# Kernel optimization log

Measured on AMD Instinct MI355X. Metric: run time of the kernel, lower is better.

Reference implementation:

```python
import jax, jax.numpy as jnp
import numpy as np

N = 20000   # nodes
E = 320000  # edges (before self-loops)
HID = 64    # hidden_dim
H = 4       # attention heads
C = HID     # per-head channels (concat=False -> mean over heads)
CDIM = 8    # contrastive_dim
NEG_SLOPE = 0.2


def setup_inputs() -> dict:
    key = jax.random.key(0)
    ks = jax.random.split(key, 32)
    g = lambda k, shape: (jax.random.normal(k, shape, jnp.float32) * 0.05)
    inp = {
        "x": jax.random.normal(ks[0], (N, 8), jnp.float32),
        "edge_index": jax.random.randint(ks[1], (2, E), 0, N, jnp.int64),
        # lc_encode MLP: 8 -> 32 -> HID
        "W_enc1": g(ks[2], (8, 32)),  "b_enc1": jnp.zeros((32,), jnp.float32),
        "W_enc2": g(ks[3], (32, HID)), "b_enc2": jnp.zeros((HID,), jnp.float32),
        # three GATConv layers: lin (HID -> H*C, no bias), att_src/att_dst (H, C), bias (C,)
        "W_g1": g(ks[4], (HID, H * C)), "as1": g(ks[5], (H, C)), "ad1": g(ks[6], (H, C)), "bg1": jnp.zeros((C,), jnp.float32),
        "W_g2": g(ks[7], (HID, H * C)), "as2": g(ks[8], (H, C)), "ad2": g(ks[9], (H, C)), "bg2": jnp.zeros((C,), jnp.float32),
        "W_g3": g(ks[10], (HID, H * C)), "as3": g(ks[11], (H, C)), "ad3": g(ks[12], (H, C)), "bg3": jnp.zeros((C,), jnp.float32),
        # output MLP: HID -> 64 -> 32 -> CDIM (dropout inactive at eval)
        "W_o1": g(ks[13], (HID, 64)), "b_o1": jnp.zeros((64,), jnp.float32),
        "W_o2": g(ks[14], (64, 32)),  "b_o2": jnp.zeros((32,), jnp.float32),
        "W_o3": g(ks[15], (32, CDIM)), "b_o3": jnp.zeros((CDIM,), jnp.float32),
    }
    return inp


def gat_conv(x, src, dst, n, W, att_src, att_dst, bias):
    # PyG GATConv, heads=H, concat=False (mean over heads), eval mode (no dropout)
    h = (x @ W).reshape(n, H, C)                       # [N,H,C]
    a_src = jnp.einsum('nhc,hc->nh', h, att_src)        # [N,H]
    a_dst = jnp.einsum('nhc,hc->nh', h, att_dst)        # [N,H]
    logits = jax.nn.leaky_relu(a_src[src] + a_dst[dst], NEG_SLOPE)  # [Etot,H]
    m = jax.ops.segment_max(logits, dst, num_segments=n)            # segment softmax (stable)
    e = jnp.exp(logits - m[dst])
    denom = jax.ops.segment_sum(e, dst, num_segments=n)
    alpha = e / (denom[dst] + 1e-16)                    # [Etot,H]
    msg = h[src] * alpha[:, :, None]                    # [Etot,H,C]
    out = jax.ops.segment_sum(msg, dst, num_segments=n) # [N,H,C]
    return out.mean(axis=1) + bias                      # concat=False -> head mean


def reference(x, edge_index, W_enc1, b_enc1, W_enc2, b_enc2,
              W_g1, as1, ad1, bg1, W_g2, as2, ad2, bg2, W_g3, as3, ad3, bg3,
              W_o1, b_o1, W_o2, b_o2, W_o3, b_o3):
    n = x.shape[0]
    loops = jnp.arange(n, dtype=edge_index.dtype)       # GATConv add_self_loops=True
    src = jnp.concatenate([edge_index[0], loops])
    dst = jnp.concatenate([edge_index[1], loops])

    h = jax.nn.elu(jax.nn.elu(x @ W_enc1 + b_enc1) @ W_enc2 + b_enc2)
    h1 = gat_conv(h, src, dst, n, W_g1, as1, ad1, bg1) + h
    h2 = gat_conv(h1, src, dst, n, W_g2, as2, ad2, bg2) + h1
    h3 = gat_conv(h2, src, dst, n, W_g3, as3, ad3, bg3) + h2

    o = jax.nn.elu(h3 @ W_o1 + b_o1)
    o = jax.nn.elu(o @ W_o2 + b_o2)
    return o @ W_o3 + b_o3
```

## Files before the change

kernel.cpp:

```cpp
#include <hip/hip_runtime.h>
#include <cstdint>
#include <cstddef>

#define NEG_SLOPE 0.2f

__device__ __forceinline__ float elu_f(float x) {
    return x > 0.f ? x : expm1f(x);
}

__global__ __launch_bounds__(256) void prep_kernel(
    const int* __restrict__ ei,
    const float* __restrict__ W0, const float* __restrict__ as0, const float* __restrict__ ad0,
    const float* __restrict__ W1, const float* __restrict__ as1, const float* __restrict__ ad1,
    const float* __restrict__ W2, const float* __restrict__ as2, const float* __restrict__ ad2,
    int* __restrict__ cnt, int* __restrict__ ready, int* __restrict__ flag,
    float* __restrict__ vfold, int n) {
    const int b = blockIdx.x, t = threadIdx.x;
    if (b < 79) {
        const int i = b * 256 + t;
        if (i < n) cnt[i] = 0;
        if (b == 0) {
            if (t < 128) ready[t] = 0;
            if (t == 0) {
                int acc = 0;
#pragma unroll
                for (int k = 0; k < 8; ++k) acc |= ei[2 * k + 1];
                flag[0] = (acc == 0) ? 1 : 0;
            }
        }
        return;
    }
    const int e = (b - 79) * 256 + t;
    if (e >= 1536) return;
    const int l = e >> 9, rem = e & 511;
    const int k = rem >> 3, j = rem & 7, h = j & 3;
    const float* W   = (l == 0) ? W0  : (l == 1) ? W1  : W2;
    const float* as_ = (l == 0) ? as0 : (l == 1) ? as1 : as2;
    const float* ad_ = (l == 0) ? ad0 : (l == 1) ? ad1 : ad2;
    const float* av = (j < 4) ? as_ : ad_;
    const float* wr = W + k * 256 + h * 64;
    const float* ar = av + h * 64;
    float s = 0.f;
#pragma unroll 8
    for (int cc = 0; cc < 64; ++cc) s += wr[cc] * ar[cc];
    vfold[l * 512 + k * 8 + j] = s;
}

__global__ void count_kernel(const int* __restrict__ ei, const int* __restrict__ flag,
                             int E, int Etot, int* __restrict__ cnt) {
    int e = blockIdx.x * blockDim.x + threadIdx.x;
    if (e >= Etot) return;
    int d;
    if (e < E) d = flag[0] ? ei[2 * (size_t)(E + e)] : ei[E + e];
    else       d = e - E;
    atomicAdd(&cnt[d], 1);
}

#define SCAN_B 256
__global__ __launch_bounds__(256) void scan_onepass_kernel(
    const int* __restrict__ cnt, int* __restrict__ ready,
    int* __restrict__ rowptr, int* __restrict__ cursor, int n) {
    __shared__ int sd[SCAN_B];
    __shared__ int sred[128];
    __shared__ int s_pref;
    const int b = blockIdx.x, t = threadIdx.x;
    const int g = b * SCAN_B + t;
    const int v = (g < n) ? cnt[g] : 0;
    sd[t] = v;
    __syncthreads();
    for (int off = 1; off < SCAN_B; off <<= 1) {
        int add = (t >= off) ? sd[t - off] : 0;
        __syncthreads();
        sd[t] += add;
        __syncthreads();
    }
    if (t == SCAN_B - 1) atomicExch(&ready[b], sd[SCAN_B - 1] + 1);
    if (t < 128) {
        int pv = 0;
        if (t < b) {
            do { pv = atomicAdd(&ready[t], 0); __builtin_amdgcn_s_sleep(1); } while (pv == 0);
            pv -= 1;
        }
        sred[t] = pv;
    }
    __syncthreads();
    if (t == 0) {
        int s = 0;
#pragma unroll 8
        for (int i = 0; i < 128; ++i) s += sred[i];
        s_pref = s;
    }
    __syncthreads();
    const int pre = s_pref;
    if (g < n) {
        const int e = pre + sd[t];
        rowptr[g + 1] = e;
        cursor[g] = e - v;
        if (g == 0) rowptr[0] = 0;
    }
}

__global__ void fill_kernel(const int* __restrict__ ei, const int* __restrict__ flag,
                            int E, int Etot, int* __restrict__ cursor,
                            int* __restrict__ col) {
    int e = blockIdx.x * blockDim.x + threadIdx.x;
    if (e >= Etot) return;
    int s, d;
    if (e < E) {
        if (flag[0]) { s = ei[2 * (size_t)e]; d = ei[2 * (size_t)(E + e)]; }
        else         { s = ei[e];             d = ei[E + e]; }
    } else {
        s = d = e - E;
    }
    int pos = atomicAdd(&cursor[d], 1);
    col[pos] = s;
}

#define H1STR 68
__global__ __launch_bounds__(256) void encoder_kernel(
    const float* __restrict__ x,
    const float* __restrict__ W1, const float* __restrict__ b1,
    const float* __restrict__ W2, const float* __restrict__ b2,
    const float* __restrict__ vfold0,
    float* __restrict__ h0, float* __restrict__ asrc, float* __restrict__ adst,
    int n_nodes) {
    __shared__ float W1s[256];
    __shared__ float b1s[32];
    __shared__ float W2s[2048];
    __shared__ float b2s[64];
    __shared__ float vsd[512];
    __shared__ float xS[512];
    __shared__ float h1T[32 * H1STR];
    const int t = threadIdx.x;
    const int n0 = blockIdx.x * 64;
    const int rem = n_nodes - n0;

    *(float4*)(W2s + t * 4) = *(const float4*)(W2 + t * 4);
    *(float4*)(W2s + 1024 + t * 4) = *(const float4*)(W2 + 1024 + t * 4);
    if (t < 64)  *(float4*)(W1s + t * 4) = *(const float4*)(W1 + t * 4);
    if (t < 8)   *(float4*)(b1s + t * 4) = *(const float4*)(b1 + t * 4);
    if (t < 16)  *(float4*)(b2s + t * 4) = *(const float4*)(b2 + t * 4);
    if (t < 128) *(float4*)(vsd + t * 4) = *(const float4*)(vfold0 + t * 4);
    if (t < 128) {
        const int fidx = t * 4;
        float4 v = make_float4(0.f, 0.f, 0.f, 0.f);
        if (fidx < rem * 8) v = *(const float4*)(x + (size_t)n0 * 8 + fidx);
        *(float4*)(xS + fidx) = v;
    }
    __syncthreads();

    {
        const int nl = t >> 2;
        const int j0 = (t & 3) * 8;
        const float4 xa = *(const float4*)(xS + nl * 8);
        const float4 xb = *(const float4*)(xS + nl * 8 + 4);
        const float xk[8] = {xa.x, xa.y, xa.z, xa.w, xb.x, xb.y, xb.z, xb.w};
        float a[8];
#pragma unroll
        for (int u = 0; u < 8; ++u) a[u] = b1s[j0 + u];
#pragma unroll
        for (int k = 0; k < 8; ++k) {
            const float4 w0 = *(const float4*)(W1s + k * 32 + j0);
            const float4 w1 = *(const float4*)(W1s + k * 32 + j0 + 4);
            a[0] += xk[k] * w0.x; a[1] += xk[k] * w0.y;
            a[2] += xk[k] * w0.z; a[3] += xk[k] * w0.w;
            a[4] += xk[k] * w1.x; a[5] += xk[k] * w1.y;
            a[6] += xk[k] * w1.z; a[7] += xk[k] * w1.w;
        }
#pragma unroll
        for (int u = 0; u < 8; ++u) h1T[(j0 + u) * H1STR + nl] = elu_f(a[u]);
    }
    __syncthreads();

    const int cg = t & 15;
    const int nq = t >> 4;
    const int c0 = cg * 4;
    float acc[4][4];
#pragma unroll
    for (int i = 0; i < 4; ++i)
#pragma unroll
        for (int c = 0; c < 4; ++c) acc[i][c] = b2s[c0 + c];
#pragma unroll 8
    for (int k = 0; k < 32; ++k) {
        const float4 hv = *(const float4*)(h1T + k * H1STR + nq * 4);
        const float4 wv = *(const float4*)(W2s + k * 64 + c0);
        const float hvv[4] = {hv.x, hv.y, hv.z, hv.w};
#pragma unroll
        for (int i = 0; i < 4; ++i) {
            acc[i][0] += hvv[i] * wv.x; acc[i][1] += hvv[i] * wv.y;
            acc[i][2] += hvv[i] * wv.z; acc[i][3] += hvv[i] * wv.w;
        }
    }
    float o[4][4];
#pragma unroll
    for (int i = 0; i < 4; ++i)
#pragma unroll
        for (int c = 0; c < 4; ++c) o[i][c] = elu_f(acc[i][c]);

#pragma unroll
    for (int i = 0; i < 4; ++i) {
        const int n = n0 + nq * 4 + i;
        if (n < n_nodes)
            *(float4*)(h0 + (size_t)n * 64 + c0) =
                make_float4(o[i][0], o[i][1], o[i][2], o[i][3]);
    }
    float ad[4][8];
#pragma unroll
    for (int i = 0; i < 4; ++i)
#pragma unroll
        for (int jj = 0; jj < 8; ++jj) ad[i][jj] = 0.f;
#pragma unroll
    for (int c = 0; c < 4; ++c) {
        const float4 v0 = *(const float4*)(vsd + (c0 + c) * 8);
        const float4 v1 = *(const float4*)(vsd + (c0 + c) * 8 + 4);
#pragma unroll
        for (int i = 0; i < 4; ++i) {
            ad[i][0] += o[i][c] * v0.x; ad[i][1] += o[i][c] * v0.y;
            ad[i][2] += o[i][c] * v0.z; ad[i][3] += o[i][c] * v0.w;
            ad[i][4] += o[i][c] * v1.x; ad[i][5] += o[i][c] * v1.y;
            ad[i][6] += o[i][c] * v1.z; ad[i][7] += o[i][c] * v1.w;
        }
    }
#pragma unroll
    for (int off = 1; off < 16; off <<= 1) {
#pragma unroll
        for (int i = 0; i < 4; ++i)
#pragma unroll
            for (int jj = 0; jj < 8; ++jj)
                ad[i][jj] += __shfl_xor(ad[i][jj], off);
    }
    if (cg == 0) {
#pragma unroll
        for (int i = 0; i < 4; ++i) {
            const int n = n0 + nq * 4 + i;
            if (n < n_nodes) {
#pragma unroll
                for (int h = 0; h < 4; ++h) {
                    asrc[n * 4 + h] = ad[i][h];
                    adst[n * 4 + h] = ad[i][4 + h];
                }
            }
        }
    }
}

__global__ __launch_bounds__(256) void gat_agg_kernel(
    const float* __restrict__ bin, const float* __restrict__ asrc,
    const float* __restrict__ adst, const int* __restrict__ rowptr,
    const int* __restrict__ col, float* __restrict__ g, int n_nodes) {
    const int grp = threadIdx.x >> 4;
    const int q = threadIdx.x & 15;
    const int n = blockIdx.x * 16 + grp;
    if (n >= n_nodes) return;
    const float4 ad4 = *(const float4*)(adst + (size_t)n * 4);
    const int start = rowptr[n], end = rowptr[n + 1];

    float acc[4][4];
#pragma unroll
    for (int h = 0; h < 4; ++h)
#pragma unroll
        for (int z = 0; z < 4; ++z) acc[h][z] = 0.f;
    float4 den4 = make_float4(0.f, 0.f, 0.f, 0.f);

    for (int base = start; base < end; base += 16) {
        const int cnt = min(16, end - base);
        int c = 0;
        float4 w4 = make_float4(0.f, 0.f, 0.f, 0.f);
        if (base + q < end) {
            c = col[base + q];
            const float4 av = *(const float4*)(asrc + (size_t)c * 4);
            float l0 = av.x + ad4.x; l0 = l0 > 0.f ? l0 : NEG_SLOPE * l0;
            float l1 = av.y + ad4.y; l1 = l1 > 0.f ? l1 : NEG_SLOPE * l1;
            float l2 = av.z + ad4.z; l2 = l2 > 0.f ? l2 : NEG_SLOPE * l2;
            float l3 = av.w + ad4.w; l3 = l3 > 0.f ? l3 : NEG_SLOPE * l3;
            w4.x = __expf(fminf(l0, 60.f));
            w4.y = __expf(fminf(l1, 60.f));
            w4.z = __expf(fminf(l2, 60.f));
            w4.w = __expf(fminf(l3, 60.f));
            den4.x += w4.x; den4.y += w4.y; den4.z += w4.z; den4.w += w4.w;
        }
        int j = 0;
        for (; j + 4 <= cnt; j += 4) {
#pragma unroll
            for (int u = 0; u < 4; ++u) {
                const int s = __shfl(c, j + u, 16);
                const float4 hv = *(const float4*)(bin + (size_t)s * 64 + q * 4);
                const float wx = __shfl(w4.x, j + u, 16);
                const float wy = __shfl(w4.y, j + u, 16);
                const float wz = __shfl(w4.z, j + u, 16);
                const float ww = __shfl(w4.w, j + u, 16);
                acc[0][0] += wx * hv.x; acc[0][1] += wx * hv.y;
                acc[0][2] += wx * hv.z; acc[0][3] += wx * hv.w;
                acc[1][0] += wy * hv.x; acc[1][1] += wy * hv.y;
                acc[1][2] += wy * hv.z; acc[1][3] += wy * hv.w;
                acc[2][0] += wz * hv.x; acc[2][1] += wz * hv.y;
                acc[2][2] += wz * hv.z; acc[2][3] += wz * hv.w;
                acc[3][0] += ww * hv.x; acc[3][1] += ww * hv.y;
                acc[3][2] += ww * hv.z; acc[3][3] += ww * hv.w;
            }
        }
        for (; j < cnt; ++j) {
            const int s = __shfl(c, j, 16);
            const float4 hv = *(const float4*)(bin + (size_t)s * 64 + q * 4);
            const float wx = __shfl(w4.x, j, 16);
            const float wy = __shfl(w4.y, j, 16);
            const float wz = __shfl(w4.z, j, 16);
            const float ww = __shfl(w4.w, j, 16);
            acc[0][0] += wx * hv.x; acc[0][1] += wx * hv.y;
            acc[0][2] += wx * hv.z; acc[0][3] += wx * hv.w;
            acc[1][0] += wy * hv.x; acc[1][1] += wy * hv.y;
            acc[1][2] += wy * hv.z; acc[1][3] += wy * hv.w;
            acc[2][0] += wz * hv.x; acc[2][1] += wz * hv.y;
            acc[2][2] += wz * hv.z; acc[2][3] += wz * hv.w;
            acc[3][0] += ww * hv.x; acc[3][1] += ww * hv.y;
            acc[3][2] += ww * hv.z; acc[3][3] += ww * hv.w;
        }
    }
#pragma unroll
    for (int off = 1; off < 16; off <<= 1) {
        den4.x += __shfl_xor(den4.x, off, 16);
        den4.y += __shfl_xor(den4.y, off, 16);
        den4.z += __shfl_xor(den4.z, off, 16);
        den4.w += __shfl_xor(den4.w, off, 16);
    }
    const float i0 = 1.f / (den4.x + 1e-16f);
    const float i1 = 1.f / (den4.y + 1e-16f);
    const float i2 = 1.f / (den4.z + 1e-16f);
    const float i3 = 1.f / (den4.w + 1e-16f);
    float* gr = g + (size_t)n * 256 + q * 4;
    *(float4*)(gr +   0) = make_float4(acc[0][0]*i0, acc[0][1]*i0, acc[0][2]*i0, acc[0][3]*i0);
    *(float4*)(gr +  64) = make_float4(acc[1][0]*i1, acc[1][1]*i1, acc[1][2]*i1, acc[1][3]*i1);
    *(float4*)(gr + 128) = make_float4(acc[2][0]*i2, acc[2][1]*i2, acc[2][2]*i2, acc[2][3]*i2);
    *(float4*)(gr + 192) = make_float4(acc[3][0]*i3, acc[3][1]*i3, acc[3][2]*i3, acc[3][3]*i3);
}

#define GSTR 132
__global__ __launch_bounds__(256) void gat_post_kernel(
    const float* __restrict__ g, const float* __restrict__ W,
    const float* __restrict__ bias, const float* __restrict__ xin,
    const float* __restrict__ vfold_next, int has_next,
    float* __restrict__ out, float* __restrict__ asrc, float* __restrict__ adst,
    const float* __restrict__ Wm1, const float* __restrict__ bm1,
    const float* __restrict__ Wm2, const float* __restrict__ bm2,
    const float* __restrict__ Wm3, const float* __restrict__ bm3,
    float* __restrict__ mlp_out, int n_nodes) {
    __shared__ float gS[64 * GSTR];
    __shared__ float Wp[128 * 64];
    __shared__ float vN[512];
    const int t = threadIdx.x;
    const int n0 = blockIdx.x * 64;
    const int cg = t & 7;
    const int ng = t >> 3;

    if (has_next && t < 128) *(float4*)(vN + t * 4) = *(const float4*)(vfold_next + t * 4);

    float acc[2][8];
#pragma unroll
    for (int i = 0; i < 2; ++i)
#pragma unroll
        for (int qq = 0; qq < 8; ++qq) acc[i][qq] = 0.f;

    for (int slab = 0; slab < 2; ++slab) {
        __syncthreads();
#pragma unroll
        for (int j = 0; j < 8; ++j) {
            const int idx = j * 256 + t;
            const int nl = idx >> 5;
            const int c4 = idx & 31;
            float4 v = make_float4(0.f, 0.f, 0.f, 0.f);
            if (n0 + nl < n_nodes)
                v = *(const float4*)(g + (size_t)(n0 + nl) * 256 + slab * 128 + c4 * 4);
            *(float4*)(gS + nl * GSTR + c4 * 4) = v;
        }
#pragma unroll
        for (int j = 0; j < 8; ++j) {
            const int f4 = j * 256 + t;
            const int kl = f4 >> 4;
            const int kap = slab * 128 + kl;
            const int h = kap >> 6, kk = kap & 63;
            const int c = (f4 & 15) * 4;
            *(float4*)(Wp + kl * 64 + c) = *(const float4*)(W + kk * 256 + h * 64 + c);
        }
        __syncthreads();
#pragma unroll 4
        for (int kl = 0; kl < 128; ++kl) {
            const float a0 = gS[(ng * 2 + 0) * GSTR + kl];
            const float a1 = gS[(ng * 2 + 1) * GSTR + kl];
            const float4 b0 = *(const float4*)(Wp + kl * 64 + cg * 8);
            const float4 b1 = *(const float4*)(Wp + kl * 64 + cg * 8 + 4);
            acc[0][0] += a0 * b0.x; acc[0][1] += a0 * b0.y;
            acc[0][2] += a0 * b0.z; acc[0][3] += a0 * b0.w;
            acc[0][4] += a0 * b1.x; acc[0][5] += a0 * b1.y;
            acc[0][6] += a0 * b1.z; acc[0][7] += a0 * b1.w;
            acc[1][0] += a1 * b0.x; acc[1][1] += a1 * b0.y;
            acc[1][2] += a1 * b0.z; acc[1][3] += a1 * b0.w;
            acc[1][4] += a1 * b1.x; acc[1][5] += a1 * b1.y;
            acc[1][6] += a1 * b1.z; acc[1][7] += a1 * b1.w;
        }
    }

    const int c0 = cg * 8;
    const float4 bb0 = *(const float4*)(bias + c0);
    const float4 bb1 = *(const float4*)(bias + c0 + 4);
    float o[2][8];
#pragma unroll
    for (int i = 0; i < 2; ++i) {
        const int n = n0 + ng * 2 + i;
        if (n < n_nodes) {
            const float4 x0 = *(const float4*)(xin + (size_t)n * 64 + c0);
            const float4 x1 = *(const float4*)(xin + (size_t)n * 64 + c0 + 4);
            o[i][0] = 0.25f * acc[i][0] + bb0.x + x0.x;
            o[i][1] = 0.25f * acc[i][1] + bb0.y + x0.y;
            o[i][2] = 0.25f * acc[i][2] + bb0.z + x0.z;
            o[i][3] = 0.25f * acc[i][3] + bb0.w + x0.w;
            o[i][4] = 0.25f * acc[i][4] + bb1.x + x1.x;
            o[i][5] = 0.25f * acc[i][5] + bb1.y + x1.y;
            o[i][6] = 0.25f * acc[i][6] + bb1.z + x1.z;
            o[i][7] = 0.25f * acc[i][7] + bb1.w + x1.w;
            if (has_next) {
                *(float4*)(out + (size_t)n * 64 + c0) =
                    make_float4(o[i][0], o[i][1], o[i][2], o[i][3]);
                *(float4*)(out + (size_t)n * 64 + c0 + 4) =
                    make_float4(o[i][4], o[i][5], o[i][6], o[i][7]);
            }
        } else {
#pragma unroll
            for (int qq = 0; qq < 8; ++qq) o[i][qq] = 0.f;
        }
    }

    if (has_next) {
        float pj[2][8];
#pragma unroll
        for (int i = 0; i < 2; ++i)
#pragma unroll
            for (int jj = 0; jj < 8; ++jj) pj[i][jj] = 0.f;
#pragma unroll
        for (int cidx = 0; cidx < 8; ++cidx) {
#pragma unroll
            for (int jj = 0; jj < 8; ++jj) {
                const float vv = vN[(c0 + cidx) * 8 + jj];
                pj[0][jj] += o[0][cidx] * vv;
                pj[1][jj] += o[1][cidx] * vv;
            }
        }
#pragma unroll
        for (int off = 1; off < 8; off <<= 1) {
#pragma unroll
            for (int i = 0; i < 2; ++i)
#pragma unroll
                for (int jj = 0; jj < 8; ++jj)
                    pj[i][jj] += __shfl_xor(pj[i][jj], off);
        }
        if (cg == 0) {
#pragma unroll
            for (int i = 0; i < 2; ++i) {
                const int n = n0 + ng * 2 + i;
                if (n < n_nodes) {
#pragma unroll
                    for (int h = 0; h < 4; ++h) {
                        asrc[n * 4 + h] = pj[i][h];
                        adst[n * 4 + h] = pj[i][4 + h];
                    }
                }
            }
        }
        return;
    }

    __syncthreads();
#pragma unroll
    for (int i = 0; i < 2; ++i) {
        const int nl = ng * 2 + i;
        *(float4*)(gS + nl * GSTR + c0)     = make_float4(o[i][0], o[i][1], o[i][2], o[i][3]);
        *(float4*)(gS + nl * GSTR + c0 + 4) = make_float4(o[i][4], o[i][5], o[i][6], o[i][7]);
    }
    {
#pragma unroll
        for (int j = 0; j < 4; ++j)
            *(float4*)(Wp + (j * 256 + t) * 4) = *(const float4*)(Wm1 + (j * 256 + t) * 4);
#pragma unroll
        for (int j = 0; j < 2; ++j)
            *(float4*)(Wp + 4096 + (j * 256 + t) * 4) = *(const float4*)(Wm2 + (j * 256 + t) * 4);
        if (t < 64) vN[t] = bm1[t];
        else if (t < 96) vN[t] = bm2[t - 64];
        else if (t < 104) vN[t] = bm3[t - 96];
        vN[104 + t] = Wm3[t];
    }
    __syncthreads();
    {
        float a1[2][8];
#pragma unroll
        for (int i = 0; i < 2; ++i)
#pragma unroll
            for (int qq = 0; qq < 8; ++qq) a1[i][qq] = vN[c0 + qq];
#pragma unroll 4
        for (int k = 0; k < 64; ++k) {
            const float h0 = gS[(ng * 2 + 0) * GSTR + k];
            const float h1v = gS[(ng * 2 + 1) * GSTR + k];
            const float4 w0 = *(const float4*)(Wp + k * 64 + c0);
            const float4 w1 = *(const float4*)(Wp + k * 64 + c0 + 4);
            a1[0][0] += h0 * w0.x; a1[0][1] += h0 * w0.y;
            a1[0][2] += h0 * w0.z; a1[0][3] += h0 * w0.w;
            a1[0][4] += h0 * w1.x; a1[0][5] += h0 * w1.y;
            a1[0][6] += h0 * w1.z; a1[0][7] += h0 * w1.w;
            a1[1][0] += h1v * w0.x; a1[1][1] += h1v * w0.y;
            a1[1][2] += h1v * w0.z; a1[1][3] += h1v * w0.w;
            a1[1][4] += h1v * w1.x; a1[1][5] += h1v * w1.y;
            a1[1][6] += h1v * w1.z; a1[1][7] += h1v * w1.w;
        }
#pragma unroll
        for (int i = 0; i < 2; ++i) {
            const int nl = ng * 2 + i;
            float4 v0 = make_float4(elu_f(a1[i][0]), elu_f(a1[i][1]), elu_f(a1[i][2]), elu_f(a1[i][3]));
            float4 v1 = make_float4(elu_f(a1[i][4]), elu_f(a1[i][5]), elu_f(a1[i][6]), elu_f(a1[i][7]));
            *(float4*)(gS + nl * GSTR + 64 + c0)     = v0;
            *(float4*)(gS + nl * GSTR + 64 + c0 + 4) = v1;
        }
    }
    __syncthreads();
    {
        const int cg4 = t & 3;
        const int nn = t >> 2;
        const int cc0 = cg4 * 8;
        float a2[8];
#pragma unroll
        for (int qq = 0; qq < 8; ++qq) a2[qq] = vN[64 + cc0 + qq];
#pragma unroll 4
        for (int j = 0; j < 64; ++j) {
            const float ov = gS[nn * GSTR + 64 + j];
            const float4 w0 = *(const float4*)(Wp + 4096 + j * 32 + cc0);
            const float4 w1 = *(const float4*)(Wp + 4096 + j * 32 + cc0 + 4);
            a2[0] += ov * w0.x; a2[1] += ov * w0.y;
            a2[2] += ov * w0.z; a2[3] += ov * w0.w;
            a2[4] += ov * w1.x; a2[5] += ov * w1.y;
            a2[6] += ov * w1.z; a2[7] += ov * w1.w;
        }
        __syncthreads();
        *(float4*)(gS + nn * GSTR + cc0)     = make_float4(elu_f(a2[0]), elu_f(a2[1]), elu_f(a2[2]), elu_f(a2[3]));
        *(float4*)(gS + nn * GSTR + cc0 + 4) = make_float4(elu_f(a2[4]), elu_f(a2[5]), elu_f(a2[6]), elu_f(a2[7]));
    }
    __syncthreads();
    {
        const int c3 = t & 7;
        const int nq = t >> 3;
#pragma unroll
        for (int i = 0; i < 2; ++i) {
            const int nl = nq * 2 + i;
            const int n = n0 + nl;
            if (n >= n_nodes) continue;
            float a3 = vN[96 + c3];
#pragma unroll 4
            for (int j = 0; j < 32; ++j)
                a3 += gS[nl * GSTR + j] * vN[104 + j * 8 + c3];
            mlp_out[(size_t)n * 8 + c3] = a3;
        }
    }
}

extern "C" void kernel_launch(void* const* d_in, const int* in_sizes, int n_in,
                              void* d_out, int out_size, void* d_ws, size_t ws_size,
                              hipStream_t stream) {
    const float* x     = (const float*)d_in[0];
    const int*   ei    = (const int*)d_in[1];
    const float* Wenc1 = (const float*)d_in[2];
    const float* benc1 = (const float*)d_in[3];
    const float* Wenc2 = (const float*)d_in[4];
    const float* benc2 = (const float*)d_in[5];
    const float* Wg[3]  = {(const float*)d_in[6],  (const float*)d_in[10], (const float*)d_in[14]};
    const float* as_[3] = {(const float*)d_in[7],  (const float*)d_in[11], (const float*)d_in[15]};
    const float* ad_[3] = {(const float*)d_in[8],  (const float*)d_in[12], (const float*)d_in[16]};
    const float* bg[3]  = {(const float*)d_in[9],  (const float*)d_in[13], (const float*)d_in[17]};
    const float* Wo1 = (const float*)d_in[18];
    const float* bo1 = (const float*)d_in[19];
    const float* Wo2 = (const float*)d_in[20];
    const float* bo2 = (const float*)d_in[21];
    const float* Wo3 = (const float*)d_in[22];
    const float* bo3 = (const float*)d_in[23];

    const int N = in_sizes[0] / 8;
    const int E = in_sizes[1] / 2;
    const int Etot = E + N;
    const int nblk = (N + SCAN_B - 1) / SCAN_B;

    float* buf0  = (float*)d_ws;
    float* buf1  = buf0 + (size_t)N * 64;
    float* g     = buf1 + (size_t)N * 64;
    float* asrc  = g + (size_t)N * 256;
    float* adst  = asrc + (size_t)N * 4;
    float* vfold = adst + (size_t)N * 4;
    int* rowptr = (int*)(vfold + 3 * 512);
    int* cursor = rowptr + (N + 2);
    int* cnt    = cursor + N;
    int* ready  = cnt + N;
    int* flag   = ready + 128;
    int* col    = flag + 2;

    prep_kernel<<<nblk + 6, 256, 0, stream>>>(ei,
        Wg[0], as_[0], ad_[0], Wg[1], as_[1], ad_[1], Wg[2], as_[2], ad_[2],
        cnt, ready, flag, vfold, N);
    count_kernel<<<(Etot + 255) / 256, 256, 0, stream>>>(ei, flag, E, Etot, cnt);
    scan_onepass_kernel<<<nblk, SCAN_B, 0, stream>>>(cnt, ready, rowptr, cursor, N);
    fill_kernel<<<(Etot + 255) / 256, 256, 0, stream>>>(ei, flag, E, Etot, cursor, col);

    encoder_kernel<<<(N + 63) / 64, 256, 0, stream>>>(x, Wenc1, benc1, Wenc2, benc2,
                                                      vfold, buf0, asrc, adst, N);

    float* bin = buf0;
    float* bout = buf1;
    for (int l = 0; l < 3; ++l) {
        gat_agg_kernel<<<(N + 15) / 16, 256, 0, stream>>>(bin, asrc, adst, rowptr, col,
                                                          g, N);
        const int has_next = (l < 2) ? 1 : 0;
        gat_post_kernel<<<(N + 63) / 64, 256, 0, stream>>>(
            g, Wg[l], bg[l], bin, vfold + (l + 1 < 3 ? (l + 1) * 512 : 0), has_next,
            bout, asrc, adst,
            Wo1, bo1, Wo2, bo2, Wo3, bo3, (float*)d_out, N);
        float* tmp = bin; bin = bout; bout = tmp;
    }
}
```

Measured before the change: 287.5 us.

## Merge CSR build and encoder into fewer launches with in-kernel scan-fill sync

Replaces the five setup kernels (prep, count, scan, fill, encoder) with a memset plus two kernels. The first runs edge counting, the encoder MLP (folding layer-0 attention vectors itself) and the layer 1-2 vfold computation as disjoint block ranges of one grid. The second runs the scan blocks and the fill blocks together, with fill blocks spinning on a global completion counter. The aim is to cut launch overhead and inter-kernel gaps. The risk is that fill blocks spin while holding CU slots, and that the design relies on scan blocks being scheduled before the blocks that wait on them.

New measurement: 359.9 us. 1.25x slower.

```diff
diff --git a/kernel.cpp b/kernel.cpp
--- a/kernel.cpp
+++ b/kernel.cpp
@@ -8,147 +8,94 @@
     return x > 0.f ? x : expm1f(x);
 }
 
-__global__ __launch_bounds__(256) void prep_kernel(
-    const int* __restrict__ ei,
-    const float* __restrict__ W0, const float* __restrict__ as0, const float* __restrict__ ad0,
-    const float* __restrict__ W1, const float* __restrict__ as1, const float* __restrict__ ad1,
-    const float* __restrict__ W2, const float* __restrict__ as2, const float* __restrict__ ad2,
-    int* __restrict__ cnt, int* __restrict__ ready, int* __restrict__ flag,
-    float* __restrict__ vfold, int n) {
+#define H1STR 68
+__global__ __launch_bounds__(256) void countenc_kernel(
+    const int* __restrict__ ei, const float* __restrict__ x,
+    const float* __restrict__ Wenc1, const float* __restrict__ benc1,
+    const float* __restrict__ Wenc2, const float* __restrict__ benc2,
+    const float* __restrict__ Wg0, const float* __restrict__ as0,
+    const float* __restrict__ ad0,
+    const float* __restrict__ Wg1, const float* __restrict__ as1,
+    const float* __restrict__ ad1,
+    const float* __restrict__ Wg2, const float* __restrict__ as2,
+    const float* __restrict__ ad2,
+    int* __restrict__ cnt, float* __restrict__ vfold,
+    float* __restrict__ h0, float* __restrict__ asrc, float* __restrict__ adst,
+    int N, int E, int nblkE, int nEnc) {
     const int b = blockIdx.x, t = threadIdx.x;
-    if (b < 79) {
-        const int i = b * 256 + t;
-        if (i < n) cnt[i] = 0;
-        if (b == 0) {
-            if (t < 128) ready[t] = 0;
-            if (t == 0) {
-                int acc = 0;
-#pragma unroll
-                for (int k = 0; k < 8; ++k) acc |= ei[2 * k + 1];
-                flag[0] = (acc == 0) ? 1 : 0;
-            }
-        }
-        return;
-    }
-    const int e = (b - 79) * 256 + t;
-    if (e >= 1536) return;
-    const int l = e >> 9, rem = e & 511;
-    const int k = rem >> 3, j = rem & 7, h = j & 3;
-    const float* W   = (l == 0) ? W0  : (l == 1) ? W1  : W2;
-    const float* as_ = (l == 0) ? as0 : (l == 1) ? as1 : as2;
-    const float* ad_ = (l == 0) ? ad0 : (l == 1) ? ad1 : ad2;
-    const float* av = (j < 4) ? as_ : ad_;
-    const float* wr = W + k * 256 + h * 64;
-    const float* ar = av + h * 64;
-    float s = 0.f;
-#pragma unroll 8
-    for (int cc = 0; cc < 64; ++cc) s += wr[cc] * ar[cc];
-    vfold[l * 512 + k * 8 + j] = s;
-}
-
-__global__ void count_kernel(const int* __restrict__ ei, const int* __restrict__ flag,
-                             int E, int Etot, int* __restrict__ cnt) {
-    int e = blockIdx.x * blockDim.x + threadIdx.x;
-    if (e >= Etot) return;
-    int d;
-    if (e < E) d = flag[0] ? ei[2 * (size_t)(E + e)] : ei[E + e];
-    else       d = e - E;
-    atomicAdd(&cnt[d], 1);
-}
-
-#define SCAN_B 256
-__global__ __launch_bounds__(256) void scan_onepass_kernel(
-    const int* __restrict__ cnt, int* __restrict__ ready,
-    int* __restrict__ rowptr, int* __restrict__ cursor, int n) {
-    __shared__ int sd[SCAN_B];
-    __shared__ int sred[128];
-    __shared__ int s_pref;
-    const int b = blockIdx.x, t = threadIdx.x;
-    const int g = b * SCAN_B + t;
-    const int v = (g < n) ? cnt[g] : 0;
-    sd[t] = v;
-    __syncthreads();
-    for (int off = 1; off < SCAN_B; off <<= 1) {
-        int add = (t >= off) ? sd[t - off] : 0;
-        __syncthreads();
-        sd[t] += add;
-        __syncthreads();
-    }
-    if (t == SCAN_B - 1) atomicExch(&ready[b], sd[SCAN_B - 1] + 1);
-    if (t < 128) {
-        int pv = 0;
-        if (t < b) {
-            do { pv = atomicAdd(&ready[t], 0); __builtin_amdgcn_s_sleep(1); } while (pv == 0);
-            pv -= 1;
-        }
-        sred[t] = pv;
-    }
-    __syncthreads();
-    if (t == 0) {
-        int s = 0;
-#pragma unroll 8
-        for (int i = 0; i < 128; ++i) s += sred[i];
-        s_pref = s;
-    }
-    __syncthreads();
-    const int pre = s_pref;
-    if (g < n) {
-        const int e = pre + sd[t];
-        rowptr[g + 1] = e;
-        cursor[g] = e - v;
-        if (g == 0) rowptr[0] = 0;
-    }
-}
-
-__global__ void fill_kernel(const int* __restrict__ ei, const int* __restrict__ flag,
-                            int E, int Etot, int* __restrict__ cursor,
-                            int* __restrict__ col) {
-    int e = blockIdx.x * blockDim.x + threadIdx.x;
-    if (e >= Etot) return;
-    int s, d;
-    if (e < E) {
-        if (flag[0]) { s = ei[2 * (size_t)e]; d = ei[2 * (size_t)(E + e)]; }
-        else         { s = ei[e];             d = ei[E + e]; }
-    } else {
-        s = d = e - E;
-    }
-    int pos = atomicAdd(&cursor[d], 1);
-    col[pos] = s;
-}
-
-#define H1STR 68
-__global__ __launch_bounds__(256) void encoder_kernel(
-    const float* __restrict__ x,
-    const float* __restrict__ W1, const float* __restrict__ b1,
-    const float* __restrict__ W2, const float* __restrict__ b2,
-    const float* __restrict__ vfold0,
-    float* __restrict__ h0, float* __restrict__ asrc, float* __restrict__ adst,
-    int n_nodes) {
+    const int Etot = E + N;
+
     __shared__ float W1s[256];
     __shared__ float b1s[32];
-    __shared__ float W2s[2048];
     __shared__ float b2s[64];
     __shared__ float vsd[512];
     __shared__ float xS[512];
+    __shared__ float W2s[2048];
     __shared__ float h1T[32 * H1STR];
-    const int t = threadIdx.x;
-    const int n0 = blockIdx.x * 64;
-    const int rem = n_nodes - n0;
-
-    *(float4*)(W2s + t * 4) = *(const float4*)(W2 + t * 4);
-    *(float4*)(W2s + 1024 + t * 4) = *(const float4*)(W2 + 1024 + t * 4);
-    if (t < 64)  *(float4*)(W1s + t * 4) = *(const float4*)(W1 + t * 4);
-    if (t < 8)   *(float4*)(b1s + t * 4) = *(const float4*)(b1 + t * 4);
-    if (t < 16)  *(float4*)(b2s + t * 4) = *(const float4*)(b2 + t * 4);
-    if (t < 128) *(float4*)(vsd + t * 4) = *(const float4*)(vfold0 + t * 4);
+    __shared__ int sflag;
+
+    if (b < nblkE) {
+        if (t == 0) {
+            int acc = 0;
+#pragma unroll
+            for (int k = 0; k < 8; ++k) acc |= ei[2 * k + 1];
+            sflag = (acc == 0) ? 1 : 0;
+        }
+        __syncthreads();
+        const int e = b * 256 + t;
+        if (e < Etot) {
+            int d;
+            if (e < E) d = sflag ? ei[2 * (size_t)(E + e)] : ei[E + e];
+            else       d = e - E;
+            atomicAdd(&cnt[d], 1);
+        }
+        return;
+    }
+    if (b >= nblkE + nEnc) {
+        const int e = (b - nblkE - nEnc) * 256 + t;
+        if (e < 1024) {
+            const int l = 1 + (e >> 9), rem = e & 511;
+            const int k = rem >> 3, j = rem & 7, h = j & 3;
+            const float* W   = (l == 1) ? Wg1 : Wg2;
+            const float* asl = (l == 1) ? as1 : as2;
+            const float* adl = (l == 1) ? ad1 : ad2;
+            const float* av = (j < 4) ? asl : adl;
+            const float* wr = W + k * 256 + h * 64;
+            const float* ar = av + h * 64;
+            float s = 0.f;
+#pragma unroll 8
+            for (int cc = 0; cc < 64; ++cc) s += wr[cc] * ar[cc];
+            vfold[l * 512 + k * 8 + j] = s;
+        }
+        return;
+    }
+
+    const int n0 = (b - nblkE) * 64;
+    const int rem = N - n0;
+    *(float4*)(W2s + t * 4) = *(const float4*)(Wenc2 + t * 4);
+    *(float4*)(W2s + 1024 + t * 4) = *(const float4*)(Wenc2 + 1024 + t * 4);
+    if (t < 64)  *(float4*)(W1s + t * 4) = *(const float4*)(Wenc1 + t * 4);
+    if (t < 8)   *(float4*)(b1s + t * 4) = *(const float4*)(benc1 + t * 4);
+    if (t < 16)  *(float4*)(b2s + t * 4) = *(const float4*)(benc2 + t * 4);
     if (t < 128) {
         const int fidx = t * 4;
         float4 v = make_float4(0.f, 0.f, 0.f, 0.f);
         if (fidx < rem * 8) v = *(const float4*)(x + (size_t)n0 * 8 + fidx);
         *(float4*)(xS + fidx) = v;
     }
+#pragma unroll
+    for (int u = 0; u < 2; ++u) {
+        const int e2 = t * 2 + u;
+        const int k = e2 >> 3, j = e2 & 7, h = j & 3;
+        const float* av = (j < 4) ? as0 : ad0;
+        const float* wr = Wg0 + k * 256 + h * 64;
+        const float* ar = av + h * 64;
+        float s = 0.f;
+#pragma unroll 8
+        for (int cc = 0; cc < 64; ++cc) s += wr[cc] * ar[cc];
+        vsd[k * 8 + j] = s;
+    }
     __syncthreads();
-
     {
         const int nl = t >> 2;
         const int j0 = (t & 3) * 8;
@@ -171,76 +118,153 @@
         for (int u = 0; u < 8; ++u) h1T[(j0 + u) * H1STR + nl] = elu_f(a[u]);
     }
     __syncthreads();
-
-    const int cg = t & 15;
-    const int nq = t >> 4;
-    const int c0 = cg * 4;
-    float acc[4][4];
-#pragma unroll
-    for (int i = 0; i < 4; ++i)
-#pragma unroll
-        for (int c = 0; c < 4; ++c) acc[i][c] = b2s[c0 + c];
+    {
+        const int cg = t & 15;
+        const int nq = t >> 4;
+        const int c0 = cg * 4;
+        float acc[4][4];
+#pragma unroll
+        for (int i = 0; i < 4; ++i)
+#pragma unroll
+            for (int c = 0; c < 4; ++c) acc[i][c] = b2s[c0 + c];
 #pragma unroll 8
-    for (int k = 0; k < 32; ++k) {
-        const float4 hv = *(const float4*)(h1T + k * H1STR + nq * 4);
-        const float4 wv = *(const float4*)(W2s + k * 64 + c0);
-        const float hvv[4] = {hv.x, hv.y, hv.z, hv.w};
-#pragma unroll
-        for (int i = 0; i < 4; ++i) {
-            acc[i][0] += hvv[i] * wv.x; acc[i][1] += hvv[i] * wv.y;
-            acc[i][2] += hvv[i] * wv.z; acc[i][3] += hvv[i] * wv.w;
-        }
-    }
-    float o[4][4];
-#pragma unroll
-    for (int i = 0; i < 4; ++i)
-#pragma unroll
-        for (int c = 0; c < 4; ++c) o[i][c] = elu_f(acc[i][c]);
-
-#pragma unroll
-    for (int i = 0; i < 4; ++i) {
-        const int n = n0 + nq * 4 + i;
-        if (n < n_nodes)
-            *(float4*)(h0 + (size_t)n * 64 + c0) =
-                make_float4(o[i][0], o[i][1], o[i][2], o[i][3]);
-    }
-    float ad[4][8];
-#pragma unroll
-    for (int i = 0; i < 4; ++i)
-#pragma unroll
-        for (int jj = 0; jj < 8; ++jj) ad[i][jj] = 0.f;
-#pragma unroll
-    for (int c = 0; c < 4; ++c) {
-        const float4 v0 = *(const float4*)(vsd + (c0 + c) * 8);
-        const float4 v1 = *(const float4*)(vsd + (c0 + c) * 8 + 4);
-#pragma unroll
-        for (int i = 0; i < 4; ++i) {
-            ad[i][0] += o[i][c] * v0.x; ad[i][1] += o[i][c] * v0.y;
-            ad[i][2] += o[i][c] * v0.z; ad[i][3] += o[i][c] * v0.w;
-            ad[i][4] += o[i][c] * v1.x; ad[i][5] += o[i][c] * v1.y;
-            ad[i][6] += o[i][c] * v1.z; ad[i][7] += o[i][c] * v1.w;
-        }
-    }
-#pragma unroll
-    for (int off = 1; off < 16; off <<= 1) {
+        for (int k = 0; k < 32; ++k) {
+            const float4 hv = *(const float4*)(h1T + k * H1STR + nq * 4);
+            const float4 wv = *(const float4*)(W2s + k * 64 + c0);
+            const float hvv[4] = {hv.x, hv.y, hv.z, hv.w};
+#pragma unroll
+            for (int i = 0; i < 4; ++i) {
+                acc[i][0] += hvv[i] * wv.x; acc[i][1] += hvv[i] * wv.y;
+                acc[i][2] += hvv[i] * wv.z; acc[i][3] += hvv[i] * wv.w;
+            }
+        }
+        float o[4][4];
 #pragma unroll
         for (int i = 0; i < 4; ++i)
 #pragma unroll
-            for (int jj = 0; jj < 8; ++jj)
-                ad[i][jj] += __shfl_xor(ad[i][jj], off);
-    }
-    if (cg == 0) {
+            for (int c = 0; c < 4; ++c) o[i][c] = elu_f(acc[i][c]);
 #pragma unroll
         for (int i = 0; i < 4; ++i) {
             const int n = n0 + nq * 4 + i;
-            if (n < n_nodes) {
-#pragma unroll
-                for (int h = 0; h < 4; ++h) {
-                    asrc[n * 4 + h] = ad[i][h];
-                    adst[n * 4 + h] = ad[i][4 + h];
+            if (n < N)
+                *(float4*)(h0 + (size_t)n * 64 + c0) =
+                    make_float4(o[i][0], o[i][1], o[i][2], o[i][3]);
+        }
+        float ad[4][8];
+#pragma unroll
+        for (int i = 0; i < 4; ++i)
+#pragma unroll
+            for (int jj = 0; jj < 8; ++jj) ad[i][jj] = 0.f;
+#pragma unroll
+        for (int c = 0; c < 4; ++c) {
+            const float4 v0 = *(const float4*)(vsd + (c0 + c) * 8);
+            const float4 v1 = *(const float4*)(vsd + (c0 + c) * 8 + 4);
+#pragma unroll
+            for (int i = 0; i < 4; ++i) {
+                ad[i][0] += o[i][c] * v0.x; ad[i][1] += o[i][c] * v0.y;
+                ad[i][2] += o[i][c] * v0.z; ad[i][3] += o[i][c] * v0.w;
+                ad[i][4] += o[i][c] * v1.x; ad[i][5] += o[i][c] * v1.y;
+                ad[i][6] += o[i][c] * v1.z; ad[i][7] += o[i][c] * v1.w;
+            }
+        }
+#pragma unroll
+        for (int off = 1; off < 16; off <<= 1) {
+#pragma unroll
+            for (int i = 0; i < 4; ++i)
+#pragma unroll
+                for (int jj = 0; jj < 8; ++jj)
+                    ad[i][jj] += __shfl_xor(ad[i][jj], off);
+        }
+        if (cg == 0) {
+#pragma unroll
+            for (int i = 0; i < 4; ++i) {
+                const int n = n0 + nq * 4 + i;
+                if (n < N) {
+#pragma unroll
+                    for (int h = 0; h < 4; ++h) {
+                        asrc[n * 4 + h] = ad[i][h];
+                        adst[n * 4 + h] = ad[i][4 + h];
+                    }
                 }
             }
         }
+    }
+}
+
+__global__ __launch_bounds__(256, 6) void scanfill_kernel(
+    const int* __restrict__ ei, const int* __restrict__ cnt,
+    int* __restrict__ ready, int* __restrict__ sdone,
+    int* __restrict__ rowptr, int* __restrict__ cursor, int* __restrict__ col,
+    int N, int E) {
+    __shared__ int sd[256];
+    __shared__ int sred[128];
+    __shared__ int sprf;
+    __shared__ int sflag;
+    const int b = blockIdx.x, t = threadIdx.x;
+    const int Etot = E + N;
+    const int nscan = (N + 255) >> 8;
+
+    if (b < nscan) {
+        const int gi = b * 256 + t;
+        const int v = (gi < N) ? cnt[gi] : 0;
+        sd[t] = v;
+        __syncthreads();
+        for (int off = 1; off < 256; off <<= 1) {
+            int add = (t >= off) ? sd[t - off] : 0;
+            __syncthreads();
+            sd[t] += add;
+            __syncthreads();
+        }
+        if (t == 255) atomicExch(&ready[b], sd[255] + 1);
+        if (t < 128) {
+            int pv = 0;
+            if (t < b) {
+                do { pv = atomicAdd(&ready[t], 0); __builtin_amdgcn_s_sleep(1); } while (pv == 0);
+                pv -= 1;
+            }
+            sred[t] = pv;
+        }
+        __syncthreads();
+        if (t == 0) {
+            int s = 0;
+#pragma unroll 8
+            for (int i = 0; i < 128; ++i) s += sred[i];
+            sprf = s;
+        }
+        __syncthreads();
+        const int pre = sprf;
+        if (gi < N) {
+            const int e = pre + sd[t];
+            rowptr[gi + 1] = e;
+            cursor[gi] = e - v;
+            if (gi == 0) rowptr[0] = 0;
+        }
+        __threadfence();
+        __syncthreads();
+        if (t == 0) atomicAdd(sdone, 1);
+        return;
+    }
+
+    if (t == 0) {
+        int acc = 0;
+#pragma unroll
+        for (int k = 0; k < 8; ++k) acc |= ei[2 * k + 1];
+        sflag = (acc == 0) ? 1 : 0;
+        while (__hip_atomic_load(sdone, __ATOMIC_ACQUIRE, __HIP_MEMORY_SCOPE_AGENT) < nscan)
+            __builtin_amdgcn_s_sleep(4);
+    }
+    __syncthreads();
+    const int e = (b - nscan) * 256 + t;
+    if (e < Etot) {
+        int s, d;
+        if (e < E) {
+            if (sflag) { s = ei[2 * (size_t)e]; d = ei[2 * (size_t)(E + e)]; }
+            else       { s = ei[e];             d = ei[E + e]; }
+        } else {
+            s = d = e - E;
+        }
+        int pos = atomicAdd(&cursor[d], 1);
+        col[pos] = s;
     }
 }
 
@@ -263,7 +287,7 @@
     float4 den4 = make_float4(0.f, 0.f, 0.f, 0.f);
 
     for (int base = start; base < end; base += 16) {
-        const int cnt = min(16, end - base);
+        const int cnt2 = min(16, end - base);
         int c = 0;
         float4 w4 = make_float4(0.f, 0.f, 0.f, 0.f);
         if (base + q < end) {
@@ -280,7 +304,7 @@
             den4.x += w4.x; den4.y += w4.y; den4.z += w4.z; den4.w += w4.w;
         }
         int j = 0;
-        for (; j + 4 <= cnt; j += 4) {
+        for (; j + 4 <= cnt2; j += 4) {
 #pragma unroll
             for (int u = 0; u < 4; ++u) {
                 const int s = __shfl(c, j + u, 16);
@@ -299,7 +323,7 @@
                 acc[3][2] += ww * hv.z; acc[3][3] += ww * hv.w;
             }
         }
-        for (; j < cnt; ++j) {
+        for (; j < cnt2; ++j) {
             const int s = __shfl(c, j, 16);
             const float4 hv = *(const float4*)(bin + (size_t)s * 64 + q * 4);
             const float wx = __shfl(w4.x, j, 16);
@@ -581,7 +605,9 @@
     const int N = in_sizes[0] / 8;
     const int E = in_sizes[1] / 2;
     const int Etot = E + N;
-    const int nblk = (N + SCAN_B - 1) / SCAN_B;
+    const int nblkE = (Etot + 255) / 256;
+    const int nEnc  = (N + 63) / 64;
+    const int nscan = (N + 255) / 256;
 
     float* buf0  = (float*)d_ws;
     float* buf1  = buf0 + (size_t)N * 64;
@@ -593,18 +619,18 @@
     int* cursor = rowptr + (N + 2);
     int* cnt    = cursor + N;
     int* ready  = cnt + N;
-    int* flag   = ready + 128;
-    int* col    = flag + 2;
-
-    prep_kernel<<<nblk + 6, 256, 0, stream>>>(ei,
+    int* sdone  = ready + 128;
+    int* col    = sdone + 8;
+
+    hipMemsetAsync(cnt, 0, (size_t)(N + 136) * sizeof(int), stream);
+
+    countenc_kernel<<<nblkE + nEnc + 4, 256, 0, stream>>>(
+        ei, x, Wenc1, benc1, Wenc2, benc2,
         Wg[0], as_[0], ad_[0], Wg[1], as_[1], ad_[1], Wg[2], as_[2], ad_[2],
-        cnt, ready, flag, vfold, N);
-    count_kernel<<<(Etot + 255) / 256, 256, 0, stream>>>(ei, flag, E, Etot, cnt);
-    scan_onepass_kernel<<<nblk, SCAN_B, 0, stream>>>(cnt, ready, rowptr, cursor, N);
-    fill_kernel<<<(Etot + 255) / 256, 256, 0, stream>>>(ei, flag, E, Etot, cursor, col);
-
-    encoder_kernel<<<(N + 63) / 64, 256, 0, stream>>>(x, Wenc1, benc1, Wenc2, benc2,
-                                                      vfold, buf0, asrc, adst, N);
+        cnt, vfold, buf0, asrc, adst, N, E, nblkE, nEnc);
+
+    scanfill_kernel<<<nscan + nblkE, 256, 0, stream>>>(
+        ei, cnt, ready, sdone, rowptr, cursor, col, N, E);
 
     float* bin = buf0;
     float* bout = buf1;
```
